# Kernel optimization log

Measured on AMD Instinct MI355X. Metric: run time of the kernel, lower is better.

## Reference

```python
import jax, jax.numpy as jnp
import numpy as np
from jax.scipy.special import logsumexp

EPSILON = 0.1
N_ITERS = 50
SIM_TEMP = 0.1
GAMMA_POS = 0.02
BARY_W = 0.5
GCOS_W = 0.2

B, N, D = 16, 1024, 256


def _normalize(x, axis=-1, eps=1e-12):
    # matches torch F.normalize: x / max(||x||, eps)
    n = jnp.linalg.norm(x, axis=axis, keepdims=True)
    return x / jnp.maximum(n, eps)


def _position_prior(n):
    idx = jnp.arange(n, dtype=jnp.float32)
    diff = (idx[:, None] - idx[None, :]) / max(n - 1, 1)
    return jnp.abs(diff)[None]  # (1, N, N), l1 metric


def _sinkhorn_log_domain(C, loga, logb, eps, n_iters):
    logK = -C / eps  # (B, N, N)
    logKT = jnp.swapaxes(logK, -1, -2)
    f0 = jnp.zeros(loga.shape, C.dtype)
    g0 = jnp.zeros(logb.shape, C.dtype)

    def step(carry, _):
        f, g = carry
        f = loga - logsumexp(logK + g[:, None, :], axis=-1)
        g = logb - logsumexp(logKT + f[:, None, :], axis=-1)
        return (f, g), None

    (f, g), _ = jax.lax.scan(step, (f0, g0), None, length=n_iters)
    logT = logK + f[:, :, None] + g[:, None, :]
    return jnp.exp(logT), logT


def setup_inputs() -> dict:
    key = jax.random.key(0)
    k1, k2 = jax.random.split(key)
    return {
        "eeg_embedding": jax.random.normal(k1, (B, N, D), jnp.float32),
        "text_embedding": jax.random.normal(k2, (B, N, D), jnp.float32),
    }


def reference(eeg_embedding, text_embedding):
    X, Y = eeg_embedding, text_embedding
    Xn = _normalize(X)
    Yn = _normalize(Y)
    b_, n_, _ = Xn.shape

    S = jnp.einsum('bnd,bmd->bnm', Xn, Yn)
    C_content = jnp.maximum(1.0 - S, 0.0) / SIM_TEMP
    C = C_content + GAMMA_POS * _position_prior(n_)

    loga = jnp.full((b_, n_), jnp.log(1.0 / n_ + 1e-12), jnp.float32)
    logb = jnp.full((b_, n_), jnp.log(1.0 / n_ + 1e-12), jnp.float32)
    T, _logT = _sinkhorn_log_domain(C, loga, logb, EPSILON, N_ITERS)

    L_main = jnp.sum(T * C_content, axis=(-1, -2))

    r = jnp.sum(T, axis=-1)[..., None]  # (B, N, 1)
    c = jnp.sum(T, axis=-2)[..., None]  # (B, N, 1)
    Y_bar = jnp.einsum('bnm,bmd->bnd', T, Y) / (r + 1e-08)
    X_bar = jnp.einsum('bmn,bmd->bnd', T, X) / (c + 1e-08)
    L_bary = jnp.mean((X - Y_bar) ** 2, axis=(1, 2)) + jnp.mean((Y - X_bar) ** 2, axis=(1, 2))

    x_g = jnp.sum(X * r, axis=1) / (jnp.sum(r, axis=1) + 1e-08)
    y_g = jnp.sum(Y * c, axis=1) / (jnp.sum(c, axis=1) + 1e-08)
    x_g = _normalize(x_g)
    y_g = _normalize(y_g)
    L_cos_global = 1.0 - jnp.sum(x_g * y_g, axis=-1)

    loss = L_main + BARY_W * L_bary + GCOS_W * L_cos_global
    return jnp.mean(loss)
```

## Files before the change

kernel.cpp:

```cpp
#include <hip/hip_runtime.h>
#include <hip/hip_fp16.h>

#define BB 16
#define NN 1024
#define DD 256
#define NSLAB 16
#define ETW 40

typedef _Float16 h8 __attribute__((ext_vector_type(8)));
typedef _Float16 hv4 __attribute__((ext_vector_type(4)));
typedef _Float16 h2 __attribute__((ext_vector_type(2)));
typedef float f32x4 __attribute__((ext_vector_type(4)));

#if __has_builtin(__builtin_amdgcn_exp2f)
#define EXP2F(x) __builtin_amdgcn_exp2f(x)
#else
#define EXP2F(x) exp2f(x)
#endif
#if __has_builtin(__builtin_amdgcn_logf)
#define LOG2F(x) __builtin_amdgcn_logf(x)
#else
#define LOG2F(x) log2f(x)
#endif

constexpr float K_A2  = -144.26950408889634f;
constexpr float CPOS2 = (float)(0.2 * 1.4426950408889634 / 1023.0);
constexpr float C1    = 0.06931471805599453f;
constexpr float BASE2 = -10.0f;
constexpr float P2B   = 0x1p-10f;

#define PIDX(i) ((i) + ((i) >> 3))

__device__ __forceinline__ float waveReduceSum(float v) {
#pragma unroll
  for (int o = 32; o; o >>= 1) v += __shfl_xor(v, o);
  return v;
}

__device__ __forceinline__ void ldsVec16p(const float* lds, int j0, float (&out)[16]) {
#pragma unroll
  for (int k = 0; k < 8; ++k) {
    out[k] = lds[PIDX(j0 + k)];
    out[8 + k] = lds[PIDX(512 + j0 + k)];
  }
}

__global__ __launch_bounds__(256) void normalize_kernel(
    const float* __restrict__ X, const float* __restrict__ Y,
    _Float16* __restrict__ Xh, _Float16* __restrict__ Yh) {
  int wave = threadIdx.x >> 6;
  int lane = threadIdx.x & 63;
  int row = blockIdx.x * 4 + wave;
  const float* src;
  _Float16* dst;
  if (row < BB * NN) { src = X + (size_t)row * DD; dst = Xh + (size_t)row * DD; }
  else { int r2 = row - BB * NN; src = Y + (size_t)r2 * DD; dst = Yh + (size_t)r2 * DD; }
  float4 v = *(const float4*)(src + lane * 4);
  float ss = v.x * v.x + v.y * v.y + v.z * v.z + v.w * v.w;
  ss = waveReduceSum(ss);
  float sc = 1.0f / fmaxf(sqrtf(ss), 1e-12f);
  hv4 hv;
  hv[0] = (_Float16)(v.x * sc); hv[1] = (_Float16)(v.y * sc);
  hv[2] = (_Float16)(v.z * sc); hv[3] = (_Float16)(v.w * sc);
  *(hv4*)(dst + lane * 4) = hv;
}

__global__ __launch_bounds__(256) void transpose_kernel(
    const float* __restrict__ X, const float* __restrict__ Y,
    _Float16* __restrict__ XT, _Float16* __restrict__ YT) {
  __shared__ _Float16 tile[64][72];
  int zb = blockIdx.z;
  const float* E;
  _Float16* ET;
  if (zb < BB) { E = X + (size_t)zb * NN * DD; ET = XT + (size_t)zb * DD * NN; }
  else { E = Y + (size_t)(zb - BB) * NN * DD; ET = YT + (size_t)(zb - BB) * DD * NN; }
  int n0 = blockIdx.x * 64, d0 = blockIdx.y * 64;
  int t = threadIdx.x;
  int lr = t >> 2, lc = (t & 3) * 16;
#pragma unroll
  for (int k = 0; k < 16; k += 4) {
    float4 v = *(const float4*)(E + (size_t)(n0 + lr) * DD + d0 + lc + k);
    tile[lc + k + 0][lr] = (_Float16)v.x;
    tile[lc + k + 1][lr] = (_Float16)v.y;
    tile[lc + k + 2][lr] = (_Float16)v.z;
    tile[lc + k + 3][lr] = (_Float16)v.w;
  }
  __syncthreads();
#pragma unroll
  for (int k = 0; k < 16; k += 8) {
    h8 o;
#pragma unroll
    for (int j = 0; j < 8; ++j) o[j] = tile[lr][lc + k + j];
    *(h8*)(ET + (size_t)(d0 + lr) * NN + n0 + lc + k) = o;
  }
}

__global__ __launch_bounds__(256) void gemm_a2_kernel(
    const _Float16* __restrict__ Xh, const _Float16* __restrict__ Yh,
    _Float16* __restrict__ A2, _Float16* __restrict__ A2T) {
  const int zb = blockIdx.z;
  const int b = zb & 15;
  const _Float16* Ah = (zb < BB) ? Xh : Yh;
  const _Float16* Bh = (zb < BB) ? Yh : Xh;
  _Float16* Out = (zb < BB) ? A2 : A2T;
  const int I0 = blockIdx.y * 128;
  const int J0 = blockIdx.x * 128;
  const int lane = threadIdx.x & 63;
  const int wave = threadIdx.x >> 6;
  const int m = lane & 15, quad = lane >> 4;
  const _Float16* Abase = Ah + ((size_t)b * NN + I0 + wave * 32) * DD;
  const _Float16* Bbase = Bh + ((size_t)b * NN + J0) * DD;
  f32x4 acc[2][8] = {};
  for (int k0 = 0; k0 < DD; k0 += 32) {
    int koff = k0 + quad * 8;
    h8 a0 = *(const h8*)(Abase + (size_t)m * DD + koff);
    h8 a1 = *(const h8*)(Abase + (size_t)(m + 16) * DD + koff);
#pragma unroll
    for (int t = 0; t < 8; ++t) {
      h8 bf = *(const h8*)(Bbase + (size_t)(t * 16 + m) * DD + koff);
      acc[0][t] = __builtin_amdgcn_mfma_f32_16x16x32_f16(a0, bf, acc[0][t], 0, 0, 0);
      acc[1][t] = __builtin_amdgcn_mfma_f32_16x16x32_f16(a1, bf, acc[1][t], 0, 0, 0);
    }
  }
  _Float16* Ob = Out + ((size_t)b * NN + I0 + wave * 32) * NN + J0;
#pragma unroll
  for (int a = 0; a < 2; ++a)
#pragma unroll
    for (int t = 0; t < 8; ++t)
#pragma unroll
      for (int r = 0; r < 4; ++r) {
        int row = a * 16 + quad * 4 + r;
        int col = t * 16 + m;
        float s = acc[a][t][r];
        float ri = (float)(I0 + wave * 32 + row);
        float ci = (float)(J0 + col);
        Ob[(size_t)row * NN + col] =
            (_Float16)(K_A2 * fmaxf(1.0f - s, 0.0f) - CPOS2 * fabsf(ri - ci));
      }
}

#define SINK_SMEM (131072 + 4608 + 256 + 256 + 256 + 256)

__device__ __forceinline__ void storePart2(float* p, float2 v) {
  union { float2 v; unsigned long long u; } cv;
  cv.v = v;
  __hip_atomic_store((unsigned long long*)p, cv.u, __ATOMIC_RELAXED,
                     __HIP_MEMORY_SCOPE_AGENT);
}

__device__ __forceinline__ float2 loadPart2(const float* p) {
  union { float2 v; unsigned long long u; } cv;
  cv.u = __hip_atomic_load((const unsigned long long*)p, __ATOMIC_RELAXED,
                           __HIP_MEMORY_SCOPE_AGENT);
  return cv.v;
}

__device__ __forceinline__ void atomAddF(float* p, float v) {
  (void)__hip_atomic_fetch_add(p, v, __ATOMIC_RELAXED, __HIP_MEMORY_SCOPE_AGENT);
}

__device__ __forceinline__ float4 loadCoh4(const float* p) {
  float4 v;
  asm volatile("global_load_dwordx4 %0, %1, off sc0 sc1\n\ts_waitcnt vmcnt(0)"
               : "=v"(v)
               : "v"(p)
               : "memory");
  return v;
}

__global__ __launch_bounds__(512) void sink_persist(
    const _Float16* __restrict__ A2, float* __restrict__ Cbuf,
    float* __restrict__ Fv, float* __restrict__ Gf,
    float* __restrict__ rOut, float* __restrict__ cOut, float* __restrict__ Lrow,
    unsigned* __restrict__ bar) {
  extern __shared__ char smem[];
  _Float16* slab = (_Float16*)smem;
  float* lv = (float*)(smem + 131072);
  float* f_l = (float*)(smem + 135680);
  float* m_l = (float*)(smem + 135936);
  float* fv_l = (float*)(smem + 136192);
  volatile unsigned* dflag = (volatile unsigned*)(smem + 136448);
  const int b = blockIdx.y;
  const int slabId = blockIdx.x;
  const int t = threadIdx.x, lane = t & 63, wave = t >> 6;
  unsigned* barB = bar + b * 16;

  const _Float16* src = A2 + ((size_t)b * NN + slabId * 64) * NN;
  for (int e = t * 8; e < 64 * NN; e += 512 * 8)
    *(h8*)(slab + e) = *(const h8*)(src + e);
  __syncthreads();

  const int j0 = lane * 8;
  const int r0w = wave * 8;

  {
    h8 qa8[8], qb8[8];
#pragma unroll
    for (int r = 0; r < 8; ++r) {
      qa8[r] = *(const h8*)(slab + (size_t)(r0w + r) * NN + j0);
      qb8[r] = *(const h8*)(slab + (size_t)(r0w + r) * NN + 512 + j0);
    }
    float mr[8];
#pragma unroll
    for (int r = 0; r < 8; ++r) {
      float m = (float)qa8[r][0];
#pragma unroll
      for (int k = 1; k < 8; ++k) m = fmaxf(m, (float)qa8[r][k]);
#pragma unroll
      for (int k = 0; k < 8; ++k) m = fmaxf(m, (float)qb8[r][k]);
      mr[r] = m;
    }
#pragma unroll
    for (int o = 32; o; o >>= 1)
#pragma unroll
      for (int r = 0; r < 8; ++r) mr[r] = fmaxf(mr[r], __shfl_xor(mr[r], o));
#pragma unroll
    for (int r = 0; r < 8; ++r) {
      h8 oa, ob;
#pragma unroll
      for (int k = 0; k < 8; ++k) {
        oa[k] = (_Float16)EXP2F((float)qa8[r][k] - mr[r]);
        ob[k] = (_Float16)EXP2F((float)qb8[r][k] - mr[r]);
      }
      *(h8*)(slab + (size_t)(r0w + r) * NN + j0) = oa;
      *(h8*)(slab + (size_t)(r0w + r) * NN + 512 + j0) = ob;
      if (lane == 0) m_l[r0w + r] = mr[r];
    }
  }

  const size_t CB = (size_t)BB * NN;
  float gv[16];

  for (int it = 0; it < 50; ++it) {
    if (it == 0) {
      lv[PIDX(2 * t)] = 1.0f;
      lv[PIDX(2 * t + 1)] = 1.0f;
    } else if (t < 256) {
      const float* Cr = Cbuf + (size_t)((it + 2) % 3) * CB + b * NN;
      float4 cc = loadCoh4(Cr + 4 * t);
      lv[PIDX(4 * t + 0)] = P2B / cc.x;
      lv[PIDX(4 * t + 1)] = P2B / cc.y;
      lv[PIDX(4 * t + 2)] = P2B / cc.z;
      lv[PIDX(4 * t + 3)] = P2B / cc.w;
    }
    if (t == 0) *dflag = 0;
    __syncthreads();
    ldsVec16p(lv, j0, gv);
    {
      float* Cz = Cbuf + (size_t)((it + 1) % 3) * CB + b * NN;
      if (t < 32) storePart2(Cz + slabId * 64 + 2 * t, make_float2(0.f, 0.f));
    }
    float sr8[8];
#pragma unroll
    for (int r = 0; r < 8; ++r) {
      h8 qa = *(const h8*)(slab + (size_t)(r0w + r) * NN + j0);
      h8 qb = *(const h8*)(slab + (size_t)(r0w + r) * NN + 512 + j0);
      float s = 0.f;
#pragma unroll
      for (int k = 0; k < 8; ++k) s = fmaf((float)qa[k], gv[k], s);
#pragma unroll
      for (int k = 0; k < 8; ++k) s = fmaf((float)qb[k], gv[8 + k], s);
      sr8[r] = s;
    }
#pragma unroll
    for (int o = 32; o; o >>= 1)
#pragma unroll
      for (int r = 0; r < 8; ++r) sr8[r] += __shfl_xor(sr8[r], o);
    if (lane == 0) {
#pragma unroll
      for (int r = 0; r < 8; ++r) {
        f_l[r0w + r] = P2B / sr8[r];
        if (it == 49) {
          float flog = BASE2 - m_l[r0w + r] - LOG2F(sr8[r]);
          fv_l[r0w + r] = flog;
          Fv[b * NN + slabId * 64 + r0w + r] = flog;
        }
      }
    }
    __syncthreads();
    float p0 = 0.f, p1 = 0.f;
    const _Float16* cp = slab + 2 * t;
#pragma unroll 4
    for (int i4 = 0; i4 < 16; ++i4) {
      float4 u4 = *(const float4*)&f_l[i4 * 4];
#pragma unroll
      for (int q = 0; q < 4; ++q) {
        h2 a = *(const h2*)(cp + (size_t)(i4 * 4 + q) * NN);
        p0 = fmaf((float)a[0], u4[q], p0);
        p1 = fmaf((float)a[1], u4[q], p1);
      }
    }
    {
      float* Ca = Cbuf + (size_t)(it % 3) * CB + b * NN;
      atomAddF(Ca + 2 * t, p0);
      atomAddF(Ca + 2 * t + 1, p1);
    }
    __syncthreads();
    if (t == 0)
      __hip_atomic_fetch_add(barB, 1u, __ATOMIC_RELAXED, __HIP_MEMORY_SCOPE_AGENT);
    if (lane == 0) {
      unsigned target = (unsigned)NSLAB * (unsigned)(it + 1);
      while (*dflag == 0) {
        unsigned v = __hip_atomic_load(barB, __ATOMIC_RELAXED,
                                       __HIP_MEMORY_SCOPE_AGENT);
        if (v >= target) { *dflag = 1; break; }
        __builtin_amdgcn_s_sleep(1);
      }
    }
    __syncthreads();
  }

  {
    const float* Cg = Cbuf + (size_t)(49 % 3) * CB + b * NN;
    float2 cc = loadPart2(Cg + 2 * t);
    float g0 = BASE2 - LOG2F(cc.x);
    float g1 = BASE2 - LOG2F(cc.y);
    lv[PIDX(2 * t)] = g0;
    lv[PIDX(2 * t + 1)] = g1;
    if (slabId == 0) {
      Gf[b * NN + 2 * t] = g0;
      Gf[b * NN + 2 * t + 1] = g1;
    }
  }
  __syncthreads();
  ldsVec16p(lv, j0, gv);

#pragma unroll
  for (int r = 0; r < 8; ++r) {
    int rl = r0w + r;
    int i = slabId * 64 + rl;
    float fi = fv_l[rl];
    const _Float16* grow = A2 + ((size_t)b * NN + i) * NN;
    h8 qa = *(const h8*)(grow + j0);
    h8 qb = *(const h8*)(grow + 512 + j0);
    float fr = (float)i;
    float sr = 0.f, sl = 0.f;
#pragma unroll
    for (int k = 0; k < 8; ++k) {
      float a2a = (float)qa[k];
      float a2b = (float)qb[k];
      float Ta = EXP2F(a2a + fi + gv[k]);
      float Tb = EXP2F(a2b + fi + gv[8 + k]);
      sr += Ta + Tb;
      float ca = a2a + CPOS2 * fabsf(fr - (float)(j0 + k));
      float cb = a2b + CPOS2 * fabsf(fr - (float)(512 + j0 + k));
      sl = fmaf(Ta, ca, sl);
      sl = fmaf(Tb, cb, sl);
    }
    sr = waveReduceSum(sr);
    sl = waveReduceSum(sl);
    if (lane == 0) {
      rOut[b * NN + i] = sr;
      cOut[b * NN + i] = EXP2F(BASE2);
      Lrow[b * NN + i] = -C1 * sl;
    }
  }
}

__global__ __launch_bounds__(256) void bary_mfma_kernel(
    const _Float16* __restrict__ A2, const _Float16* __restrict__ A2T,
    const float* __restrict__ F, const float* __restrict__ G,
    const float* __restrict__ r, const float* __restrict__ c,
    const _Float16* __restrict__ XT, const _Float16* __restrict__ YT,
    const float* __restrict__ X, const float* __restrict__ Y,
    float* __restrict__ baryA, float* __restrict__ baryB) {
  __shared__ float gl[NN];
  __shared__ float red[4];
  __shared__ _Float16 etile[2][256 * ETW];
  int id = blockIdx.x + blockIdx.y * gridDim.x + blockIdx.z * gridDim.x * gridDim.y;
  int w = (id >> 3) + (id & 7) * 64;
  const int I0 = (w & 15) * 64;
  const int bz = w >> 4;
  const int b = bz & 15;
  const int z = bz >> 4;
  const _Float16* P = z ? A2T : A2;
  const float* rowv = z ? G : F;
  const float* colv = z ? F : G;
  const float* denom = z ? c : r;
  const _Float16* EmbT = z ? XT : YT;
  const float* Ref = z ? Y : X;
  float* baryAcc = z ? baryB : baryA;
  const int t = threadIdx.x, lane = t & 63, wave = t >> 6;
  const int m = lane & 15, quad = lane >> 4;
  gl[t] = colv[b * NN + t];
  gl[t + 256] = colv[b * NN + t + 256];
  gl[t + 512] = colv[b * NN + t + 512];
  gl[t + 768] = colv[b * NN + t + 768];
  const int row = I0 + wave * 16 + m;
  const float fi = rowv[b * NN + row] + 10.0f;
  const _Float16* Pr = P + (size_t)b * NN * NN + (size_t)row * NN + quad * 8;
  const _Float16* ET = EmbT + (size_t)b * DD * NN;

  auto stageET = [&](int buf, int kc) {
#pragma unroll
    for (int i = 0; i < 4; ++i) {
      int rr = (t >> 2) + i * 64;
      int ch = t & 3;
      h8 v = *(const h8*)(ET + (size_t)rr * NN + kc + ch * 8);
      *(h8*)(&etile[buf][rr * ETW + ch * 8]) = v;
    }
  };

  f32x4 acc[16];
#pragma unroll
  for (int i = 0; i < 16; ++i) acc[i] = (f32x4){0.f, 0.f, 0.f, 0.f};
  stageET(0, 0);
  h8 a2v = *(const h8*)(Pr);
  __syncthreads();
  int buf = 0;
  for (int kc = 0; kc < NN; kc += 32) {
    const int kn = kc + 32;
    if (kn < NN) stageET(buf ^ 1, kn);
    h8 a2n = a2v;
    if (kn < NN) a2n = *(const h8*)(Pr + kn);
    float4 g0 = *(const float4*)&gl[kc + quad * 8];
    float4 g1 = *(const float4*)&gl[kc + quad * 8 + 4];
    h8 af;
    af[0] = (_Float16)EXP2F((float)a2v[0] + fi + g0.x);
    af[1] = (_Float16)EXP2F((float)a2v[1] + fi + g0.y);
    af[2] = (_Float16)EXP2F((float)a2v[2] + fi + g0.z);
    af[3] = (_Float16)EXP2F((float)a2v[3] + fi + g0.w);
    af[4] = (_Float16)EXP2F((float)a2v[4] + fi + g1.x);
    af[5] = (_Float16)EXP2F((float)a2v[5] + fi + g1.y);
    af[6] = (_Float16)EXP2F((float)a2v[6] + fi + g1.z);
    af[7] = (_Float16)EXP2F((float)a2v[7] + fi + g1.w);
#pragma unroll
    for (int nt = 0; nt < 16; ++nt) {
      h8 bf = *(const h8*)(&etile[buf][(nt * 16 + m) * ETW + quad * 8]);
      acc[nt] = __builtin_amdgcn_mfma_f32_16x16x32_f16(af, bf, acc[nt], 0, 0, 0);
    }
    a2v = a2n;
    __syncthreads();
    buf ^= 1;
  }
  float vs = 0.f;
#pragma unroll
  for (int r4 = 0; r4 < 4; ++r4) {
    int iabs = I0 + wave * 16 + quad * 4 + r4;
    float inv = 1.0f / (1024.0f * (denom[b * NN + iabs] + 1e-8f));
    const float* Rrow = Ref + ((size_t)b * NN + iabs) * DD;
#pragma unroll
    for (int nt = 0; nt < 16; ++nt) {
      int d = nt * 16 + m;
      float val = Rrow[d] - acc[nt][r4] * inv;
      vs = fmaf(val, val, vs);
    }
  }
  vs = waveReduceSum(vs);
  if (lane == 0) red[wave] = vs;
  __syncthreads();
  if (t == 0) atomicAdd(baryAcc + b, red[0] + red[1] + red[2] + red[3]);
}

__global__ __launch_bounds__(256) void xg_kernel(
    const float* __restrict__ X, const float* __restrict__ Y,
    const float* __restrict__ r, const float* __restrict__ c,
    float* __restrict__ xgp, float* __restrict__ ygp) {
  const int b = blockIdx.y, seg = blockIdx.x, d = threadIdx.x;
  float ax = 0.f, ay = 0.f;
  for (int ii = 0; ii < 256; ++ii) {
    int i = seg * 256 + ii;
    float rvv = r[b * NN + i];
    float cvv = c[b * NN + i];
    ax = fmaf(X[((size_t)b * NN + i) * DD + d], rvv, ax);
    ay = fmaf(Y[((size_t)b * NN + i) * DD + d], cvv, ay);
  }
  xgp[(size_t)(b * 4 + seg) * DD + d] = ax;
  ygp[(size_t)(b * 4 + seg) * DD + d] = ay;
}

__global__ __launch_bounds__(256) void finalize_batch(
    const float* __restrict__ r, const float* __restrict__ c,
    const float* __restrict__ Lrow, const float* __restrict__ xgp,
    const float* __restrict__ ygp, const float* __restrict__ baryA,
    const float* __restrict__ baryB, float* __restrict__ lossArr) {
  const int b = blockIdx.x;
  const int t = threadIdx.x;
  __shared__ float sd[256];
  auto bsum = [&](float v) -> float {
    sd[t] = v; __syncthreads();
    for (int o = 128; o; o >>= 1) { if (t < o) sd[t] += sd[t + o]; __syncthreads(); }
    float res = sd[0]; __syncthreads();
    return res;
  };
  float vr = 0.f, vc = 0.f, vl = 0.f;
  for (int k = 0; k < 4; ++k) {
    int i = t + 256 * k;
    vr += r[b * NN + i];
    vc += c[b * NN + i];
    vl += Lrow[b * NN + i];
  }
  float sumR = bsum(vr);
  float sumC = bsum(vc);
  float Lmain = bsum(vl);
  float xg = (xgp[(size_t)(b * 4 + 0) * DD + t] + xgp[(size_t)(b * 4 + 1) * DD + t] +
              xgp[(size_t)(b * 4 + 2) * DD + t] + xgp[(size_t)(b * 4 + 3) * DD + t]) /
             (sumR + 1e-8f);
  float yg = (ygp[(size_t)(b * 4 + 0) * DD + t] + ygp[(size_t)(b * 4 + 1) * DD + t] +
              ygp[(size_t)(b * 4 + 2) * DD + t] + ygp[(size_t)(b * 4 + 3) * DD + t]) /
             (sumC + 1e-8f);
  float nx = bsum(xg * xg);
  float ny = bsum(yg * yg);
  float dt = bsum(xg * yg);
  if (t == 0) {
    float mx = fmaxf(sqrtf(nx), 1e-12f);
    float my = fmaxf(sqrtf(ny), 1e-12f);
    float cosv = dt / (mx * my);
    float lb = (baryA[b] + baryB[b]) * (1.0f / ((float)NN * (float)DD));
    lossArr[b] = Lmain + 0.5f * lb + 0.2f * (1.0f - cosv);
  }
}

__global__ void final_mean(const float* __restrict__ lossArr, float* __restrict__ out) {
  int t = threadIdx.x;
  float v = (t < BB) ? lossArr[t] : 0.f;
  v = waveReduceSum(v);
  if (t == 0) out[0] = v * (1.0f / BB);
}

extern "C" void kernel_launch(void* const* d_in, const int* in_sizes, int n_in,
                              void* d_out, int out_size, void* d_ws, size_t ws_size,
                              hipStream_t stream) {
  const float* X = (const float*)d_in[0];
  const float* Y = (const float*)d_in[1];
  float* out = (float*)d_out;
  char* ws = (char*)d_ws;
  size_t off = 0;
  auto take = [&](size_t bytes) -> char* {
    char* p = ws + off;
    off = (off + bytes + 255) & ~(size_t)255;
    return p;
  };
  _Float16* Xh = (_Float16*)take((size_t)BB * NN * DD * 2);
  _Float16* Yh = (_Float16*)take((size_t)BB * NN * DD * 2);
  _Float16* XT_h = (_Float16*)take((size_t)BB * DD * NN * 2);
  _Float16* YT_h = (_Float16*)take((size_t)BB * DD * NN * 2);
  _Float16* A2 = (_Float16*)take((size_t)BB * NN * NN * 2);
  _Float16* A2T = (_Float16*)take((size_t)BB * NN * NN * 2);
  size_t zstart = off;
  float* Cbuf = (float*)take((size_t)3 * BB * NN * 4);
  float* baryA = (float*)take(64);
  float* baryB = (float*)take(64);
  unsigned* bar = (unsigned*)take((size_t)BB * 16 * 4);
  size_t zlen = off - zstart;
  float* Fv = (float*)take((size_t)BB * NN * 4);
  float* Gf = (float*)take((size_t)BB * NN * 4);
  float* r = (float*)take((size_t)BB * NN * 4);
  float* c = (float*)take((size_t)BB * NN * 4);
  float* Lrow = (float*)take((size_t)BB * NN * 4);
  float* xgp = (float*)take((size_t)BB * 4 * DD * 4);
  float* ygp = (float*)take((size_t)BB * 4 * DD * 4);
  float* lossArr = (float*)take(64);
  (void)in_sizes; (void)n_in; (void)out_size; (void)ws_size;

  (void)hipMemsetAsync(ws + zstart, 0, zlen, stream);

  normalize_kernel<<<dim3(2 * BB * NN / 4), dim3(256), 0, stream>>>(X, Y, Xh, Yh);
  transpose_kernel<<<dim3(NN / 64, DD / 64, 2 * BB), dim3(256), 0, stream>>>(X, Y, XT_h,
                                                                             YT_h);
  gemm_a2_kernel<<<dim3(NN / 128, NN / 128, 2 * BB), dim3(256), 0, stream>>>(Xh, Yh, A2,
                                                                             A2T);
  (void)hipFuncSetAttribute(reinterpret_cast<const void*>(sink_persist),
                            hipFuncAttributeMaxDynamicSharedMemorySize, SINK_SMEM);
  {
    void* args[] = {(void*)&A2, (void*)&Cbuf, (void*)&Fv, (void*)&Gf,
                    (void*)&r,  (void*)&c,    (void*)&Lrow, (void*)&bar};
    hipError_t lerr = hipLaunchCooperativeKernel(
        reinterpret_cast<void*>(sink_persist), dim3(NSLAB, BB), dim3(512), args,
        SINK_SMEM, stream);
    if (lerr != hipSuccess) {
      sink_persist<<<dim3(NSLAB, BB), dim3(512), SINK_SMEM, stream>>>(
          A2, Cbuf, Fv, Gf, r, c, Lrow, bar);
    }
  }
  bary_mfma_kernel<<<dim3(NN / 64, BB, 2), dim3(256), 0, stream>>>(
      A2, A2T, Fv, Gf, r, c, XT_h, YT_h, X, Y, baryA, baryB);
  xg_kernel<<<dim3(4, BB), dim3(256), 0, stream>>>(X, Y, r, c, xgp, ygp);
  finalize_batch<<<dim3(BB), dim3(256), 0, stream>>>(r, c, Lrow, xgp, ygp, baryA, baryB,
                                                     lossArr);
  final_mean<<<dim3(1), dim3(64), 0, stream>>>(lossArr, out);
}
```

Baseline: 546.7 us.

## Interleave two batches per persistent Sinkhorn block to hide barrier latency

Each persistent block now owns 32-row slabs from two different batches instead of one 64-row slab. It alternates Sinkhorn half-steps between them, so one batch's cross-block barrier wait can overlap with compute on the other. The grid becomes 32x8 blocks, and the barrier wait moves to the start of the next phase instead of the end of the current one. This adds per-phase syncthreads and raises the per-batch barrier fan-in to 32 blocks, which may increase atomic contention.

Result: slower. 668.7 us (+22.3%).

```diff
diff --git a/kernel.cpp b/kernel.cpp
--- a/kernel.cpp
+++ b/kernel.cpp
@@ -4,7 +4,7 @@
 #define BB 16
 #define NN 1024
 #define DD 256
-#define NSLAB 16
+#define NSLAB2 32
 #define ETW 40
 
 typedef _Float16 h8 __attribute__((ext_vector_type(8)));
@@ -139,7 +139,7 @@
       }
 }
 
-#define SINK_SMEM (131072 + 4608 + 256 + 256 + 256 + 256)
+#define SINK_SMEM 141312
 
 __device__ __forceinline__ void storePart2(float* p, float2 v) {
   union { float2 v; unsigned long long u; } cv;
@@ -174,35 +174,41 @@
     float* __restrict__ rOut, float* __restrict__ cOut, float* __restrict__ Lrow,
     unsigned* __restrict__ bar) {
   extern __shared__ char smem[];
-  _Float16* slab = (_Float16*)smem;
-  float* lv = (float*)(smem + 131072);
-  float* f_l = (float*)(smem + 135680);
-  float* m_l = (float*)(smem + 135936);
-  float* fv_l = (float*)(smem + 136192);
-  volatile unsigned* dflag = (volatile unsigned*)(smem + 136448);
-  const int b = blockIdx.y;
+  _Float16* slabB = (_Float16*)smem;
+  float* lvB = (float*)(smem + 131072);
+  float* f_lB = (float*)(smem + 140288);
+  float* m_lB = (float*)(smem + 140544);
+  float* fv_lB = (float*)(smem + 140800);
   const int slabId = blockIdx.x;
+  const int p = blockIdx.y;
   const int t = threadIdx.x, lane = t & 63, wave = t >> 6;
-  unsigned* barB = bar + b * 16;
-
-  const _Float16* src = A2 + ((size_t)b * NN + slabId * 64) * NN;
-  for (int e = t * 8; e < 64 * NN; e += 512 * 8)
-    *(h8*)(slab + e) = *(const h8*)(src + e);
+  const int j0 = lane * 8;
+  const int r0w = wave * 4;
+  const size_t CB = (size_t)BB * NN;
+
+#pragma unroll
+  for (int sel = 0; sel < 2; ++sel) {
+    const int bsel = 2 * p + sel;
+    const _Float16* src = A2 + ((size_t)bsel * NN + slabId * 32) * NN;
+    _Float16* slab = slabB + sel * 32 * NN;
+    for (int e = t * 8; e < 32 * NN; e += 512 * 8)
+      *(h8*)(slab + e) = *(const h8*)(src + e);
+  }
   __syncthreads();
 
-  const int j0 = lane * 8;
-  const int r0w = wave * 8;
-
-  {
-    h8 qa8[8], qb8[8];
-#pragma unroll
-    for (int r = 0; r < 8; ++r) {
+#pragma unroll
+  for (int sel = 0; sel < 2; ++sel) {
+    _Float16* slab = slabB + sel * 32 * NN;
+    float* m_l = m_lB + sel * 32;
+    h8 qa8[4], qb8[4];
+#pragma unroll
+    for (int r = 0; r < 4; ++r) {
       qa8[r] = *(const h8*)(slab + (size_t)(r0w + r) * NN + j0);
       qb8[r] = *(const h8*)(slab + (size_t)(r0w + r) * NN + 512 + j0);
     }
-    float mr[8];
-#pragma unroll
-    for (int r = 0; r < 8; ++r) {
+    float mr[4];
+#pragma unroll
+    for (int r = 0; r < 4; ++r) {
       float m = (float)qa8[r][0];
 #pragma unroll
       for (int k = 1; k < 8; ++k) m = fmaxf(m, (float)qa8[r][k]);
@@ -213,9 +219,9 @@
 #pragma unroll
     for (int o = 32; o; o >>= 1)
 #pragma unroll
-      for (int r = 0; r < 8; ++r) mr[r] = fmaxf(mr[r], __shfl_xor(mr[r], o));
-#pragma unroll
-    for (int r = 0; r < 8; ++r) {
+      for (int r = 0; r < 4; ++r) mr[r] = fmaxf(mr[r], __shfl_xor(mr[r], o));
+#pragma unroll
+    for (int r = 0; r < 4; ++r) {
       h8 oa, ob;
 #pragma unroll
       for (int k = 0; k < 8; ++k) {
@@ -228,31 +234,46 @@
     }
   }
 
-  const size_t CB = (size_t)BB * NN;
-  float gv[16];
-
-  for (int it = 0; it < 50; ++it) {
+  auto phase = [&](int sel, int it) {
+    const int bsel = 2 * p + sel;
+    _Float16* slab = slabB + sel * 32 * NN;
+    float* lv = lvB + sel * 1152;
+    float* f_l = f_lB + sel * 32;
+    float* m_l = m_lB + sel * 32;
+    float* fv_l = fv_lB + sel * 32;
+    unsigned* barB = bar + bsel * 16;
     if (it == 0) {
-      lv[PIDX(2 * t)] = 1.0f;
-      lv[PIDX(2 * t + 1)] = 1.0f;
-    } else if (t < 256) {
-      const float* Cr = Cbuf + (size_t)((it + 2) % 3) * CB + b * NN;
-      float4 cc = loadCoh4(Cr + 4 * t);
-      lv[PIDX(4 * t + 0)] = P2B / cc.x;
-      lv[PIDX(4 * t + 1)] = P2B / cc.y;
-      lv[PIDX(4 * t + 2)] = P2B / cc.z;
-      lv[PIDX(4 * t + 3)] = P2B / cc.w;
-    }
-    if (t == 0) *dflag = 0;
+      if (t < 256) {
+#pragma unroll
+        for (int k = 0; k < 4; ++k) lv[PIDX(4 * t + k)] = 1.0f;
+      }
+    } else {
+      if (lane == 0) {
+        unsigned target = (unsigned)NSLAB2 * (unsigned)it;
+        while (__hip_atomic_load(barB, __ATOMIC_RELAXED,
+                                 __HIP_MEMORY_SCOPE_AGENT) < target)
+          __builtin_amdgcn_s_sleep(1);
+      }
+      __syncthreads();
+      if (t < 256) {
+        const float* Cr = Cbuf + (size_t)((it + 2) % 3) * CB + bsel * NN;
+        float4 cc = loadCoh4(Cr + 4 * t);
+        lv[PIDX(4 * t + 0)] = P2B / cc.x;
+        lv[PIDX(4 * t + 1)] = P2B / cc.y;
+        lv[PIDX(4 * t + 2)] = P2B / cc.z;
+        lv[PIDX(4 * t + 3)] = P2B / cc.w;
+      }
+    }
     __syncthreads();
+    float gv[16];
     ldsVec16p(lv, j0, gv);
     {
-      float* Cz = Cbuf + (size_t)((it + 1) % 3) * CB + b * NN;
-      if (t < 32) storePart2(Cz + slabId * 64 + 2 * t, make_float2(0.f, 0.f));
-    }
-    float sr8[8];
-#pragma unroll
-    for (int r = 0; r < 8; ++r) {
+      float* Cz = Cbuf + (size_t)((it + 1) % 3) * CB + bsel * NN;
+      if (t < 16) storePart2(Cz + slabId * 32 + 2 * t, make_float2(0.f, 0.f));
+    }
+    float sr4[4];
+#pragma unroll
+    for (int r = 0; r < 4; ++r) {
       h8 qa = *(const h8*)(slab + (size_t)(r0w + r) * NN + j0);
       h8 qb = *(const h8*)(slab + (size_t)(r0w + r) * NN + 512 + j0);
       float s = 0.f;
@@ -260,20 +281,20 @@
       for (int k = 0; k < 8; ++k) s = fmaf((float)qa[k], gv[k], s);
 #pragma unroll
       for (int k = 0; k < 8; ++k) s = fmaf((float)qb[k], gv[8 + k], s);
-      sr8[r] = s;
+      sr4[r] = s;
     }
 #pragma unroll
     for (int o = 32; o; o >>= 1)
 #pragma unroll
-      for (int r = 0; r < 8; ++r) sr8[r] += __shfl_xor(sr8[r], o);
+      for (int r = 0; r < 4; ++r) sr4[r] += __shfl_xor(sr4[r], o);
     if (lane == 0) {
 #pragma unroll
-      for (int r = 0; r < 8; ++r) {
-        f_l[r0w + r] = P2B / sr8[r];
+      for (int r = 0; r < 4; ++r) {
+        f_l[r0w + r] = P2B / sr4[r];
         if (it == 49) {
-          float flog = BASE2 - m_l[r0w + r] - LOG2F(sr8[r]);
+          float flog = BASE2 - m_l[r0w + r] - LOG2F(sr4[r]);
           fv_l[r0w + r] = flog;
-          Fv[b * NN + slabId * 64 + r0w + r] = flog;
+          Fv[bsel * NN + slabId * 32 + r0w + r] = flog;
         }
       }
     }
@@ -281,7 +302,7 @@
     float p0 = 0.f, p1 = 0.f;
     const _Float16* cp = slab + 2 * t;
 #pragma unroll 4
-    for (int i4 = 0; i4 < 16; ++i4) {
+    for (int i4 = 0; i4 < 8; ++i4) {
       float4 u4 = *(const float4*)&f_l[i4 * 4];
 #pragma unroll
       for (int q = 0; q < 4; ++q) {
@@ -291,69 +312,80 @@
       }
     }
     {
-      float* Ca = Cbuf + (size_t)(it % 3) * CB + b * NN;
+      float* Ca = Cbuf + (size_t)(it % 3) * CB + bsel * NN;
       atomAddF(Ca + 2 * t, p0);
       atomAddF(Ca + 2 * t + 1, p1);
     }
     __syncthreads();
     if (t == 0)
-      __hip_atomic_fetch_add(barB, 1u, __ATOMIC_RELAXED, __HIP_MEMORY_SCOPE_AGENT);
+      (void)__hip_atomic_fetch_add(barB, 1u, __ATOMIC_RELAXED,
+                                   __HIP_MEMORY_SCOPE_AGENT);
+  };
+
+  for (int it = 0; it < 50; ++it) {
+    phase(0, it);
+    phase(1, it);
+  }
+
+#pragma unroll
+  for (int sel = 0; sel < 2; ++sel) {
+    const int bsel = 2 * p + sel;
+    float* lv = lvB + sel * 1152;
+    float* fv_l = fv_lB + sel * 32;
+    unsigned* barB = bar + bsel * 16;
     if (lane == 0) {
-      unsigned target = (unsigned)NSLAB * (unsigned)(it + 1);
-      while (*dflag == 0) {
-        unsigned v = __hip_atomic_load(barB, __ATOMIC_RELAXED,
-                                       __HIP_MEMORY_SCOPE_AGENT);
-        if (v >= target) { *dflag = 1; break; }
+      while (__hip_atomic_load(barB, __ATOMIC_RELAXED,
+                               __HIP_MEMORY_SCOPE_AGENT) <
+             (unsigned)NSLAB2 * 50u)
         __builtin_amdgcn_s_sleep(1);
-      }
     }
     __syncthreads();
-  }
-
-  {
-    const float* Cg = Cbuf + (size_t)(49 % 3) * CB + b * NN;
-    float2 cc = loadPart2(Cg + 2 * t);
-    float g0 = BASE2 - LOG2F(cc.x);
-    float g1 = BASE2 - LOG2F(cc.y);
-    lv[PIDX(2 * t)] = g0;
-    lv[PIDX(2 * t + 1)] = g1;
-    if (slabId == 0) {
-      Gf[b * NN + 2 * t] = g0;
-      Gf[b * NN + 2 * t + 1] = g1;
-    }
-  }
-  __syncthreads();
-  ldsVec16p(lv, j0, gv);
-
-#pragma unroll
-  for (int r = 0; r < 8; ++r) {
-    int rl = r0w + r;
-    int i = slabId * 64 + rl;
-    float fi = fv_l[rl];
-    const _Float16* grow = A2 + ((size_t)b * NN + i) * NN;
-    h8 qa = *(const h8*)(grow + j0);
-    h8 qb = *(const h8*)(grow + 512 + j0);
-    float fr = (float)i;
-    float sr = 0.f, sl = 0.f;
-#pragma unroll
-    for (int k = 0; k < 8; ++k) {
-      float a2a = (float)qa[k];
-      float a2b = (float)qb[k];
-      float Ta = EXP2F(a2a + fi + gv[k]);
-      float Tb = EXP2F(a2b + fi + gv[8 + k]);
-      sr += Ta + Tb;
-      float ca = a2a + CPOS2 * fabsf(fr - (float)(j0 + k));
-      float cb = a2b + CPOS2 * fabsf(fr - (float)(512 + j0 + k));
-      sl = fmaf(Ta, ca, sl);
-      sl = fmaf(Tb, cb, sl);
-    }
-    sr = waveReduceSum(sr);
-    sl = waveReduceSum(sl);
-    if (lane == 0) {
-      rOut[b * NN + i] = sr;
-      cOut[b * NN + i] = EXP2F(BASE2);
-      Lrow[b * NN + i] = -C1 * sl;
-    }
+    {
+      const float* Cg = Cbuf + (size_t)(49 % 3) * CB + bsel * NN;
+      float2 cc = loadPart2(Cg + 2 * t);
+      float g0 = BASE2 - LOG2F(cc.x);
+      float g1 = BASE2 - LOG2F(cc.y);
+      lv[PIDX(2 * t)] = g0;
+      lv[PIDX(2 * t + 1)] = g1;
+      if (slabId == 0) {
+        Gf[bsel * NN + 2 * t] = g0;
+        Gf[bsel * NN + 2 * t + 1] = g1;
+      }
+    }
+    __syncthreads();
+    float gv[16];
+    ldsVec16p(lv, j0, gv);
+#pragma unroll
+    for (int r = 0; r < 4; ++r) {
+      int rl = r0w + r;
+      int i = slabId * 32 + rl;
+      float fi = fv_l[rl];
+      const _Float16* grow = A2 + ((size_t)bsel * NN + i) * NN;
+      h8 qa = *(const h8*)(grow + j0);
+      h8 qb = *(const h8*)(grow + 512 + j0);
+      float fr = (float)i;
+      float sr = 0.f, sl = 0.f;
+#pragma unroll
+      for (int k = 0; k < 8; ++k) {
+        float a2a = (float)qa[k];
+        float a2b = (float)qb[k];
+        float Ta = EXP2F(a2a + fi + gv[k]);
+        float Tb = EXP2F(a2b + fi + gv[8 + k]);
+        sr += Ta + Tb;
+        float ca = a2a + CPOS2 * fabsf(fr - (float)(j0 + k));
+        float cb = a2b + CPOS2 * fabsf(fr - (float)(512 + j0 + k));
+        sl = fmaf(Ta, ca, sl);
+        sl = fmaf(Tb, cb, sl);
+      }
+      sr = waveReduceSum(sr);
+      sl = waveReduceSum(sl);
+      if (lane == 0) {
+        rOut[bsel * NN + i] = sr;
+        cOut[bsel * NN + i] = EXP2F(BASE2);
+        Lrow[bsel * NN + i] = -C1 * sl;
+      }
+    }
+    __syncthreads();
   }
 }
 
@@ -566,10 +598,10 @@
     void* args[] = {(void*)&A2, (void*)&Cbuf, (void*)&Fv, (void*)&Gf,
                     (void*)&r,  (void*)&c,    (void*)&Lrow, (void*)&bar};
     hipError_t lerr = hipLaunchCooperativeKernel(
-        reinterpret_cast<void*>(sink_persist), dim3(NSLAB, BB), dim3(512), args,
+        reinterpret_cast<void*>(sink_persist), dim3(NSLAB2, BB / 2), dim3(512), args,
         SINK_SMEM, stream);
     if (lerr != hipSuccess) {
-      sink_persist<<<dim3(NSLAB, BB), dim3(512), SINK_SMEM, stream>>>(
+      sink_persist<<<dim3(NSLAB2, BB / 2), dim3(512), SINK_SMEM, stream>>>(
           A2, Cbuf, Fv, Gf, r, c, Lrow, bar);
     }
   }
```

## Compute A2 once per tile and write transpose via LDS; drop cooperative launch

Applied to the files above, without the earlier changes.

The GEMM kernel now computes each 128x128 cost tile once, stages it in shared memory, and writes both A2 and its transpose A2T with vectorized 16-byte stores. Before, it ran a second full GEMM for the transpose and used scalar strided fp16 stores. This halves the MFMA work and improves store coalescing, at the cost of about 34KB of LDS per block and one barrier. The Sinkhorn persistent kernel is now launched with a normal launch instead of hipLaunchCooperativeKernel, which removes cooperative-launch overhead but no longer guarantees that all blocks are co-resident for its grid barrier.

Result: faster. 494.4 us, median of 2 (-9.6%).

```diff
diff --git a/kernel.cpp b/kernel.cpp
--- a/kernel.cpp
+++ b/kernel.cpp
@@ -98,18 +98,15 @@
 __global__ __launch_bounds__(256) void gemm_a2_kernel(
     const _Float16* __restrict__ Xh, const _Float16* __restrict__ Yh,
     _Float16* __restrict__ A2, _Float16* __restrict__ A2T) {
-  const int zb = blockIdx.z;
-  const int b = zb & 15;
-  const _Float16* Ah = (zb < BB) ? Xh : Yh;
-  const _Float16* Bh = (zb < BB) ? Yh : Xh;
-  _Float16* Out = (zb < BB) ? A2 : A2T;
+  __shared__ _Float16 tile[128][136];
+  const int b = blockIdx.z;
   const int I0 = blockIdx.y * 128;
   const int J0 = blockIdx.x * 128;
   const int lane = threadIdx.x & 63;
   const int wave = threadIdx.x >> 6;
   const int m = lane & 15, quad = lane >> 4;
-  const _Float16* Abase = Ah + ((size_t)b * NN + I0 + wave * 32) * DD;
-  const _Float16* Bbase = Bh + ((size_t)b * NN + J0) * DD;
+  const _Float16* Abase = Xh + ((size_t)b * NN + I0 + wave * 32) * DD;
+  const _Float16* Bbase = Yh + ((size_t)b * NN + J0) * DD;
   f32x4 acc[2][8] = {};
   for (int k0 = 0; k0 < DD; k0 += 32) {
     int koff = k0 + quad * 8;
@@ -122,21 +119,46 @@
       acc[1][t] = __builtin_amdgcn_mfma_f32_16x16x32_f16(a1, bf, acc[1][t], 0, 0, 0);
     }
   }
-  _Float16* Ob = Out + ((size_t)b * NN + I0 + wave * 32) * NN + J0;
 #pragma unroll
   for (int a = 0; a < 2; ++a)
 #pragma unroll
     for (int t = 0; t < 8; ++t)
 #pragma unroll
       for (int r = 0; r < 4; ++r) {
-        int row = a * 16 + quad * 4 + r;
+        int row = wave * 32 + a * 16 + quad * 4 + r;
         int col = t * 16 + m;
         float s = acc[a][t][r];
-        float ri = (float)(I0 + wave * 32 + row);
+        float ri = (float)(I0 + row);
         float ci = (float)(J0 + col);
-        Ob[(size_t)row * NN + col] =
+        tile[row][col] =
             (_Float16)(K_A2 * fmaxf(1.0f - s, 0.0f) - CPOS2 * fabsf(ri - ci));
       }
+  __syncthreads();
+  const int t = threadIdx.x;
+  {
+    int rr = t >> 1;
+    _Float16* Orow = A2 + ((size_t)b * NN + I0 + rr) * NN + J0;
+#pragma unroll
+    for (int i = 0; i < 8; ++i) {
+      int cc = ((t & 1) * 8 + i) * 8;
+      h8 o;
+#pragma unroll
+      for (int j = 0; j < 8; ++j) o[j] = tile[rr][cc + j];
+      *(h8*)(Orow + cc) = o;
+    }
+  }
+  {
+    int ch = t & 15;
+    int crb = t >> 4;
+#pragma unroll
+    for (int i = 0; i < 8; ++i) {
+      int cr = crb + i * 16;
+      h8 o;
+#pragma unroll
+      for (int j = 0; j < 8; ++j) o[j] = tile[ch * 8 + j][cr];
+      *(h8*)(A2T + ((size_t)b * NN + J0 + cr) * NN + I0 + ch * 8) = o;
+    }
+  }
 }
 
 #define SINK_SMEM (131072 + 4608 + 256 + 256 + 256 + 256)
@@ -558,21 +580,12 @@
   normalize_kernel<<<dim3(2 * BB * NN / 4), dim3(256), 0, stream>>>(X, Y, Xh, Yh);
   transpose_kernel<<<dim3(NN / 64, DD / 64, 2 * BB), dim3(256), 0, stream>>>(X, Y, XT_h,
                                                                              YT_h);
-  gemm_a2_kernel<<<dim3(NN / 128, NN / 128, 2 * BB), dim3(256), 0, stream>>>(Xh, Yh, A2,
-                                                                             A2T);
+  gemm_a2_kernel<<<dim3(NN / 128, NN / 128, BB), dim3(256), 0, stream>>>(Xh, Yh, A2,
+                                                                         A2T);
   (void)hipFuncSetAttribute(reinterpret_cast<const void*>(sink_persist),
                             hipFuncAttributeMaxDynamicSharedMemorySize, SINK_SMEM);
-  {
-    void* args[] = {(void*)&A2, (void*)&Cbuf, (void*)&Fv, (void*)&Gf,
-                    (void*)&r,  (void*)&c,    (void*)&Lrow, (void*)&bar};
-    hipError_t lerr = hipLaunchCooperativeKernel(
-        reinterpret_cast<void*>(sink_persist), dim3(NSLAB, BB), dim3(512), args,
-        SINK_SMEM, stream);
-    if (lerr != hipSuccess) {
-      sink_persist<<<dim3(NSLAB, BB), dim3(512), SINK_SMEM, stream>>>(
-          A2, Cbuf, Fv, Gf, r, c, Lrow, bar);
-    }
-  }
+  sink_persist<<<dim3(NSLAB, BB), dim3(512), SINK_SMEM, stream>>>(A2, Cbuf, Fv, Gf, r,
+                                                                  c, Lrow, bar);
   bary_mfma_kernel<<<dim3(NN / 64, BB, 2), dim3(256), 0, stream>>>(
       A2, A2T, Fv, Gf, r, c, XT_h, YT_h, X, Y, baryA, baryB);
   xg_kernel<<<dim3(4, BB), dim3(256), 0, stream>>>(X, Y, r, c, xgp, ygp);
```
